# Optimization experiments

Measured on AMD Instinct MI355X. Metric: run time of the kernel, lower is better.

Reference implementation:

```python
import math
import jax, jax.numpy as jnp
import numpy as np

NUM_SPECIES = 4
RCR = 5.2
RCA = 3.5
ETA_R = 16.0
ETA_A = 8.0
ZETA = 32.0
SHFR = jnp.linspace(0.9, 5.2, 17)[:-1]                      # (16,) radial shifts
SHFA = jnp.linspace(0.9, 3.5, 5)[:-1]                       # (4,) angular dist shifts
SHFZ = jnp.linspace(0.0, math.pi, 9)[:-1] + math.pi / 16.0  # (8,) angle shifts
NUM_PAIRS = NUM_SPECIES * (NUM_SPECIES + 1) // 2            # 10 species pairs


def _triu_index(num_species):
    # symmetric map (s1, s2) -> index of unordered species pair (torchani get_triu_index)
    s1, s2 = np.triu_indices(num_species)
    ret = np.zeros((num_species, num_species), dtype=np.int32)
    ret[s1, s2] = np.arange(len(s1))
    ret[s2, s1] = np.arange(len(s1))
    return jnp.asarray(ret)

TRIU = _triu_index(NUM_SPECIES)


def _cutoff_cosine(d, rc):
    return 0.5 * jnp.cos(d * (math.pi / rc)) + 0.5


def _aev(species, coordinates):
    # species: (N,A) int, -1 = padding; coordinates: (N,A,3) float
    N, A = species.shape
    valid = species >= 0
    # diff[n,i,j] = r_i - r_j  (vector from neighbor j to atom i)
    diff = coordinates[:, :, None, :] - coordinates[:, None, :, :]   # (N,A,A,3)
    d2 = jnp.sum(diff * diff, axis=-1)                               # (N,A,A)
    eye = jnp.eye(A, dtype=bool)
    pair_ok = valid[:, :, None] & valid[:, None, :] & ~eye
    d = jnp.sqrt(jnp.where(d2 > 0, d2, 1.0))                         # safe norm (masked below)

    # ---------------- radial sub-AEV ----------------
    rmask = pair_ok & (d <= RCR)
    fc_r = _cutoff_cosine(d, RCR)
    rad = 0.25 * jnp.exp(-ETA_R * (d[..., None] - SHFR) ** 2) * fc_r[..., None]  # (N,A,A,16)
    rad = jnp.where(rmask[..., None], rad, 0.0)
    onehot_s = jax.nn.one_hot(species, NUM_SPECIES, dtype=rad.dtype)             # (N,A,S)
    radial_aev = jnp.einsum('nijf,njs->nisf', rad, onehot_s)                     # scatter-add by neighbor species
    radial_aev = radial_aev.reshape(N, A, NUM_SPECIES * SHFR.shape[0])           # (N,A,64)

    # ---------------- angular sub-AEV ----------------
    amask = pair_ok & (d <= RCA)                                     # neighbor within Rca of center
    jlk = jnp.triu(jnp.ones((A, A), dtype=bool), k=1)                # unordered pair j<k
    tmask = amask[:, :, :, None] & amask[:, :, None, :] & jlk[None, None]        # (N,A,A,A) [n,i,j,k]
    # angle at center i between (r_j - r_i) and (r_k - r_i): sign cancels using diff = r_i - r_j
    dot = jnp.einsum('nijc,nikc->nijk', diff, diff)                  # (N,A,A,A)
    denom = jnp.maximum(d[:, :, :, None] * d[:, :, None, :], 1e-10)
    angles = jnp.arccos(0.95 * (dot / denom))
    fcj = _cutoff_cosine(d, RCA)
    fc_prod = fcj[:, :, :, None] * fcj[:, :, None, :]
    dsum_half = 0.5 * (d[:, :, :, None] + d[:, :, None, :])
    factor1 = ((1.0 + jnp.cos(angles[..., None] - SHFZ)) * 0.5) ** ZETA          # (N,A,A,A,8)
    factor2 = jnp.exp(-ETA_A * (dsum_half[..., None] - SHFA) ** 2)               # (N,A,A,A,4)
    terms = 2.0 * factor2[..., :, None] * factor1[..., None, :] * fc_prod[..., None, None]  # (N,A,A,A,4,8)
    terms = jnp.where(tmask[..., None, None], terms, 0.0)
    terms = terms.reshape(N, A, A, A, SHFA.shape[0] * SHFZ.shape[0])             # (N,A,A,A,32), ShfA outer / ShfZ inner
    pair_idx = TRIU[species[:, :, None], species[:, None, :]]                    # (N,A,A)
    pair_onehot = jax.nn.one_hot(pair_idx, NUM_PAIRS, dtype=terms.dtype)         # (N,A,A,P)
    angular_aev = jnp.einsum('nijkf,njkp->nipf', terms, pair_onehot)             # scatter-add by species pair
    angular_aev = angular_aev.reshape(N, A, NUM_PAIRS * SHFA.shape[0] * SHFZ.shape[0])  # (N,A,320)

    return jnp.concatenate([radial_aev, angular_aev], axis=-1)      # (N,A,384)


def setup_inputs() -> dict:
    key = jax.random.key(0)
    k1, k2 = jax.random.split(key)
    N, A = 32, 48
    species = jax.random.randint(k1, (N, A), 0, NUM_SPECIES)
    # atoms uniformly placed in a 10 Angstrom box -> realistic mix of in/out-of-cutoff pairs
    coordinates = jax.random.uniform(k2, (N, A, 3), dtype=jnp.float32) * 10.0
    return {"species": species, "coordinates": coordinates}


def reference(species, coordinates):
    return _aev(species, coordinates)
```

## Files before the change

### kernel.cpp

```cpp
#include <hip/hip_runtime.h>
#include <math.h>

#define A_ATOMS 48
#define BLK     128
#define RADLEN  64
#define ANGLEN  320
#define RCR_F 5.2f
#define RCA_F 3.5f

__device__ __constant__ float COSZ[8] = {
     0.98078528f,  0.83146961f,  0.55557023f,  0.19509032f,
    -0.19509032f, -0.55557023f, -0.83146961f, -0.98078528f};
__device__ __constant__ float SINZ[8] = {
     0.19509032f,  0.55557023f,  0.83146961f,  0.98078528f,
     0.98078528f,  0.83146961f,  0.55557023f,  0.19509032f};

__global__ __launch_bounds__(BLK) void aev_kernel(const int* __restrict__ species,
                                                  const float* __restrict__ coords,
                                                  float* __restrict__ out) {
    const int blk = blockIdx.x;
    const int n = blk / A_ATOMS;
    const int i = blk - n * A_ATOMS;
    const int tid = threadIdx.x;

    __shared__ float sx[A_ATOMS], sy[A_ATOMS], sz_[A_ATOMS];
    __shared__ int   sspec[A_ATOMS];
    __shared__ int   rr_cnt, nb_cnt;
    __shared__ float rr_d[A_ATOMS], rr_fc[A_ATOMS];
    __shared__ int   rr_s[A_ATOMS];
    __shared__ float nb_dx[A_ATOMS], nb_dy[A_ATOMS], nb_dz[A_ATOMS];
    __shared__ float nb_d[A_ATOMS], nb_fc[A_ATOMS];
    __shared__ int   nb_s[A_ATOMS];
    __shared__ float pr_x[BLK], pr_sn[BLK], pr_dh[BLK], pr_b2[BLK];
    __shared__ int   pr_pi[BLK];

    if (tid < A_ATOMS) {
        const float* c = coords + ((size_t)n * A_ATOMS + tid) * 3;
        sx[tid]  = c[0];
        sy[tid]  = c[1];
        sz_[tid] = c[2];
        sspec[tid] = species[n * A_ATOMS + tid];
    }
    if (tid == 0) { rr_cnt = 0; nb_cnt = 0; }
    __syncthreads();

    const float xi = sx[i], yi = sy[i], zi = sz_[i];
    const bool  vi = (sspec[i] >= 0);

    if (tid < A_ATOMS) {
        const int j = tid;
        if (vi && j != i && sspec[j] >= 0) {
            float dx = xi - sx[j], dy = yi - sy[j], dz = zi - sz_[j];
            float d2 = dx*dx + dy*dy + dz*dz;
            float d  = (d2 > 0.f) ? sqrtf(d2) : 1.0f;
            if (d <= RCR_F) {
                int s = atomicAdd(&rr_cnt, 1);
                rr_d[s]  = d;
                rr_fc[s] = 0.25f * (0.5f * __cosf(d * (float)(M_PI / 5.2)) + 0.5f);
                rr_s[s]  = sspec[j];
            }
            if (d <= RCA_F) {
                int s = atomicAdd(&nb_cnt, 1);
                nb_dx[s] = dx; nb_dy[s] = dy; nb_dz[s] = dz;
                nb_d[s]  = d;
                nb_fc[s] = 0.5f * __cosf(d * (float)(M_PI / 3.5)) + 0.5f;
                nb_s[s]  = sspec[j];
            }
        }
    }
    __syncthreads();

    float* o = out + (size_t)blk * (RADLEN + ANGLEN);

    if (tid < RADLEN) {
        const int   s    = tid >> 4;
        const float shfr = 0.9f + 0.26875f * (float)(tid & 15);
        float acc = 0.f;
        const int Mr = rr_cnt;
        for (int m = 0; m < Mr; ++m) {
            if (rr_s[m] == s) {
                float e = rr_d[m] - shfr;
                acc += rr_fc[m] * __expf(-16.f * e * e);
            }
        }
        o[tid] = acc;
    }

    float accf[3] = {0.f, 0.f, 0.f};
    int   pik[3];
    float czk[3], szk[3], shk[3];
    #pragma unroll
    for (int k = 0; k < 3; ++k) {
        int f = tid * 3 + k;
        if (f < ANGLEN) {
            pik[k] = f >> 5;
            int aa = (f >> 3) & 3, zz = f & 7;
            czk[k] = COSZ[zz]; szk[k] = SINZ[zz];
            shk[k] = 0.9f + 0.65f * (float)aa;
        } else {
            pik[k] = -1; czk[k] = 0.f; szk[k] = 0.f; shk[k] = 0.f;
        }
    }

    const int M = nb_cnt;
    const int P = (M * (M - 1)) >> 1;
    for (int pb = 0; pb < P; pb += BLK) {
        const int p = pb + tid;
        if (p < P) {
            int a = (int)((1.f + sqrtf(1.f + 8.f * (float)p)) * 0.5f);
            while ((a * (a - 1)) / 2 > p) --a;
            while (((a + 1) * a) / 2 <= p) ++a;
            const int b = p - (a * (a - 1)) / 2;

            const float dj = nb_d[a], dk = nb_d[b];
            const float dotp = nb_dx[a]*nb_dx[b] + nb_dy[a]*nb_dy[b] + nb_dz[a]*nb_dz[b];
            const float x  = 0.95f * dotp / fmaxf(dj * dk, 1e-10f);
            pr_x[tid]  = x;
            pr_sn[tid] = sqrtf(fmaxf(0.f, 1.f - x * x));
            pr_dh[tid] = 0.5f * (dj + dk);
            pr_b2[tid] = 2.f * nb_fc[a] * nb_fc[b];
            const int sj = nb_s[a], sk = nb_s[b];
            const int lo = (sj < sk) ? sj : sk;
            const int hi = (sj < sk) ? sk : sj;
            pr_pi[tid] = (lo * (9 - lo)) / 2 + (hi - lo);
        }
        __syncthreads();
        const int cnt = (P - pb < BLK) ? (P - pb) : BLK;
        for (int m = 0; m < cnt; ++m) {
            const float x  = pr_x[m];
            const float sn = pr_sn[m];
            const float dh = pr_dh[m];
            const float b2 = pr_b2[m];
            const int   pi = pr_pi[m];
            #pragma unroll
            for (int k = 0; k < 3; ++k) {
                if (pi == pik[k]) {
                    float c = x * czk[k] + sn * szk[k];
                    float t = 0.5f * (1.f + c);
                    float t2 = t*t, t4 = t2*t2, t8 = t4*t4, t16 = t8*t8;
                    float e = dh - shk[k];
                    accf[k] += b2 * __expf(-8.f * e * e) * (t16 * t16);
                }
            }
        }
        __syncthreads();
    }

    #pragma unroll
    for (int k = 0; k < 3; ++k) {
        int f = tid * 3 + k;
        if (f < ANGLEN) o[RADLEN + f] = accf[k];
    }
}

extern "C" void kernel_launch(void* const* d_in, const int* in_sizes, int n_in,
                              void* d_out, int out_size, void* d_ws, size_t ws_size,
                              hipStream_t stream) {
    const int*   species = (const int*)d_in[0];
    const float* coords  = (const float*)d_in[1];
    float*       out     = (float*)d_out;
    const int NA = in_sizes[0];
    aev_kernel<<<dim3(NA), dim3(BLK), 0, stream>>>(species, coords, out);
}
```

Measured before the change: 77.21 us.

## Scatter angular pair terms via shared-memory atomics instead of masked feature scan

Replaces the per-feature scan over all triplet pairs, where each thread tests every pair against its own species-pair index, with a direct scatter. Each 32-lane group takes one pair, computes the 32 shift terms for it, and atomically adds them into a shared 320-entry accumulator. This removes the wasted iterations over pairs that belong to other species pairs, along with the staging barriers. It adds contention from shared-memory float atomics. Neighbor vectors are packed into float4, and the radial work moves to the upper 64 threads.

```diff
diff --git a/kernel.cpp b/kernel.cpp
--- a/kernel.cpp
+++ b/kernel.cpp
@@ -5,15 +5,6 @@
 #define BLK     128
 #define RADLEN  64
 #define ANGLEN  320
-#define RCR_F 5.2f
-#define RCA_F 3.5f
-
-__device__ __constant__ float COSZ[8] = {
-     0.98078528f,  0.83146961f,  0.55557023f,  0.19509032f,
-    -0.19509032f, -0.55557023f, -0.83146961f, -0.98078528f};
-__device__ __constant__ float SINZ[8] = {
-     0.19509032f,  0.55557023f,  0.83146961f,  0.98078528f,
-     0.98078528f,  0.83146961f,  0.55557023f,  0.19509032f};
 
 __global__ __launch_bounds__(BLK) void aev_kernel(const int* __restrict__ species,
                                                   const float* __restrict__ coords,
@@ -28,11 +19,10 @@
     __shared__ int   rr_cnt, nb_cnt;
     __shared__ float rr_d[A_ATOMS], rr_fc[A_ATOMS];
     __shared__ int   rr_s[A_ATOMS];
-    __shared__ float nb_dx[A_ATOMS], nb_dy[A_ATOMS], nb_dz[A_ATOMS];
-    __shared__ float nb_d[A_ATOMS], nb_fc[A_ATOMS];
-    __shared__ int   nb_s[A_ATOMS];
-    __shared__ float pr_x[BLK], pr_sn[BLK], pr_dh[BLK], pr_b2[BLK];
-    __shared__ int   pr_pi[BLK];
+    __shared__ float4 nb_v[A_ATOMS];
+    __shared__ float  nb_fc[A_ATOMS];
+    __shared__ int    nb_s[A_ATOMS];
+    __shared__ float  afeat[ANGLEN];
 
     if (tid < A_ATOMS) {
         const float* c = coords + ((size_t)n * A_ATOMS + tid) * 3;
@@ -41,6 +31,7 @@
         sz_[tid] = c[2];
         sspec[tid] = species[n * A_ATOMS + tid];
     }
+    for (int t = tid; t < ANGLEN; t += BLK) afeat[t] = 0.f;
     if (tid == 0) { rr_cnt = 0; nb_cnt = 0; }
     __syncthreads();
 
@@ -53,16 +44,15 @@
             float dx = xi - sx[j], dy = yi - sy[j], dz = zi - sz_[j];
             float d2 = dx*dx + dy*dy + dz*dz;
             float d  = (d2 > 0.f) ? sqrtf(d2) : 1.0f;
-            if (d <= RCR_F) {
+            if (d <= 5.2f) {
                 int s = atomicAdd(&rr_cnt, 1);
                 rr_d[s]  = d;
                 rr_fc[s] = 0.25f * (0.5f * __cosf(d * (float)(M_PI / 5.2)) + 0.5f);
                 rr_s[s]  = sspec[j];
             }
-            if (d <= RCA_F) {
+            if (d <= 3.5f) {
                 int s = atomicAdd(&nb_cnt, 1);
-                nb_dx[s] = dx; nb_dy[s] = dy; nb_dz[s] = dz;
-                nb_d[s]  = d;
+                nb_v[s]  = make_float4(dx, dy, dz, d);
                 nb_fc[s] = 0.5f * __cosf(d * (float)(M_PI / 3.5)) + 0.5f;
                 nb_s[s]  = sspec[j];
             }
@@ -72,9 +62,10 @@
 
     float* o = out + (size_t)blk * (RADLEN + ANGLEN);
 
-    if (tid < RADLEN) {
-        const int   s    = tid >> 4;
-        const float shfr = 0.9f + 0.26875f * (float)(tid & 15);
+    if (tid >= 64) {
+        const int bin = tid - 64;
+        const int s   = bin >> 4;
+        const float shfr = 0.9f + 0.26875f * (float)(bin & 15);
         float acc = 0.f;
         const int Mr = rr_cnt;
         for (int m = 0; m < Mr; ++m) {
@@ -83,74 +74,46 @@
                 acc += rr_fc[m] * __expf(-16.f * e * e);
             }
         }
-        o[tid] = acc;
+        o[bin] = acc;
     }
 
-    float accf[3] = {0.f, 0.f, 0.f};
-    int   pik[3];
-    float czk[3], szk[3], shk[3];
-    #pragma unroll
-    for (int k = 0; k < 3; ++k) {
-        int f = tid * 3 + k;
-        if (f < ANGLEN) {
-            pik[k] = f >> 5;
-            int aa = (f >> 3) & 3, zz = f & 7;
-            czk[k] = COSZ[zz]; szk[k] = SINZ[zz];
-            shk[k] = 0.9f + 0.65f * (float)aa;
-        } else {
-            pik[k] = -1; czk[k] = 0.f; szk[k] = 0.f; shk[k] = 0.f;
-        }
-    }
+    const int ff = tid & 31;
+    const int zz = ff & 7, aa = ff >> 3;
+    float cz, szn;
+    __sincosf((float)zz * (float)(M_PI / 8.0) + (float)(M_PI / 16.0), &szn, &cz);
+    const float shfa = 0.9f + 0.65f * (float)aa;
 
     const int M = nb_cnt;
     const int P = (M * (M - 1)) >> 1;
-    for (int pb = 0; pb < P; pb += BLK) {
-        const int p = pb + tid;
-        if (p < P) {
-            int a = (int)((1.f + sqrtf(1.f + 8.f * (float)p)) * 0.5f);
-            while ((a * (a - 1)) / 2 > p) --a;
-            while (((a + 1) * a) / 2 <= p) ++a;
-            const int b = p - (a * (a - 1)) / 2;
+    const int h = tid >> 5;
+    for (int p = h; p < P; p += 4) {
+        int a = (int)((1.f + sqrtf((float)(1 + 8 * p))) * 0.5f);
+        if ((a * (a - 1)) / 2 > p) --a;
+        if (((a + 1) * a) / 2 <= p) ++a;
+        const int b = p - (a * (a - 1)) / 2;
 
-            const float dj = nb_d[a], dk = nb_d[b];
-            const float dotp = nb_dx[a]*nb_dx[b] + nb_dy[a]*nb_dy[b] + nb_dz[a]*nb_dz[b];
-            const float x  = 0.95f * dotp / fmaxf(dj * dk, 1e-10f);
-            pr_x[tid]  = x;
-            pr_sn[tid] = sqrtf(fmaxf(0.f, 1.f - x * x));
-            pr_dh[tid] = 0.5f * (dj + dk);
-            pr_b2[tid] = 2.f * nb_fc[a] * nb_fc[b];
-            const int sj = nb_s[a], sk = nb_s[b];
-            const int lo = (sj < sk) ? sj : sk;
-            const int hi = (sj < sk) ? sk : sj;
-            pr_pi[tid] = (lo * (9 - lo)) / 2 + (hi - lo);
-        }
-        __syncthreads();
-        const int cnt = (P - pb < BLK) ? (P - pb) : BLK;
-        for (int m = 0; m < cnt; ++m) {
-            const float x  = pr_x[m];
-            const float sn = pr_sn[m];
-            const float dh = pr_dh[m];
-            const float b2 = pr_b2[m];
-            const int   pi = pr_pi[m];
-            #pragma unroll
-            for (int k = 0; k < 3; ++k) {
-                if (pi == pik[k]) {
-                    float c = x * czk[k] + sn * szk[k];
-                    float t = 0.5f * (1.f + c);
-                    float t2 = t*t, t4 = t2*t2, t8 = t4*t4, t16 = t8*t8;
-                    float e = dh - shk[k];
-                    accf[k] += b2 * __expf(-8.f * e * e) * (t16 * t16);
-                }
-            }
-        }
-        __syncthreads();
+        const float4 va = nb_v[a], vb = nb_v[b];
+        const float dj = va.w, dk = vb.w;
+        const float dotp = va.x*vb.x + va.y*vb.y + va.z*vb.z;
+        const float x  = 0.95f * dotp / fmaxf(dj * dk, 1e-10f);
+        const float sn = sqrtf(fmaxf(0.f, 1.f - x * x));
+        const float dh = 0.5f * (dj + dk);
+        const float b2 = 2.f * nb_fc[a] * nb_fc[b];
+        const int sj = nb_s[a], sk = nb_s[b];
+        const int lo = (sj < sk) ? sj : sk;
+        const int hi = (sj < sk) ? sk : sj;
+        const int pidx = (lo * (9 - lo)) / 2 + (hi - lo);
+
+        const float c = x * cz + sn * szn;
+        const float t = 0.5f + 0.5f * c;
+        const float t2 = t*t, t4 = t2*t2, t8 = t4*t4, t16 = t8*t8;
+        const float e = dh - shfa;
+        const float val = b2 * __expf(-8.f * e * e) * (t16 * t16);
+        atomicAdd(&afeat[pidx * 32 + ff], val);
     }
+    __syncthreads();
 
-    #pragma unroll
-    for (int k = 0; k < 3; ++k) {
-        int f = tid * 3 + k;
-        if (f < ANGLEN) o[RADLEN + f] = accf[k];
-    }
+    for (int t = tid; t < ANGLEN; t += BLK) o[RADLEN + t] = afeat[t];
 }
 
 extern "C" void kernel_launch(void* const* d_in, const int* in_sizes, int n_in,
```

New measurement: 70.33 us. 8.9% less time.
